# Optimization experiments

Measured on AMD Instinct MI355X. Metric: run time of the kernel, lower is better.

## Reference

```python
import jax, jax.numpy as jnp
import numpy as np

N = 50000      # nodes
E = 800000     # edges
D = 256        # hidden_dim (input node features)
A = 128        # attention_dim = attention_ratio * heads
H = 8          # heads
DK = A // H    # 16


def setup_inputs() -> dict:
    key = jax.random.key(0)
    ks = jax.random.split(key, 6)
    x = jax.random.normal(ks[0], (N, D), dtype=jnp.float32)
    # small weight scale keeps exp(pre) well-conditioned (module uses tiny const init)
    Wq = jax.random.normal(ks[1], (A, D), dtype=jnp.float32) * 0.02
    bq = jnp.full((A,), 0.01, dtype=jnp.float32)
    Wk = jax.random.normal(ks[2], (A, D), dtype=jnp.float32) * 0.02
    bk = jnp.full((A,), 0.01, dtype=jnp.float32)
    edge_index = jax.random.randint(ks[3], (2, E), 0, N, dtype=jnp.int32)
    # d0_index[1] holds the two node indices each duplicated edge score scatters to
    d0_index = jax.random.randint(ks[4], (2, 2 * E), 0, N, dtype=jnp.int32)
    return {"x": x, "Wq": Wq, "bq": bq, "Wk": Wk, "bk": bk,
            "edge_index": edge_index, "d0_index": d0_index}


def reference(x, Wq, bq, Wk, bk, edge_index, d0_index):
    # linear projections -> [N, H, DK]
    q = (x @ Wq.T + bq).reshape(N, H, DK)
    k = (x @ Wk.T + bk).reshape(N, H, DK)
    src, dst = edge_index[0], edge_index[1]
    q_i = q[src]   # [E, H, DK]
    k_j = k[dst]
    q_j = q[dst]
    k_i = k[src]
    # symmetrized scaled-dot attention score per edge/head
    pre = 0.5 * jnp.sum(q_i * k_j + q_j * k_i, axis=-1)  # [E, H]
    pre = jnp.mean(pre, axis=-1)                          # [E]
    diagA1 = jnp.exp(pre)
    # duplicate each edge score: (a, a, b, b, ...) == torch (view(-1,1)*ones(E,2)).view(-1)
    edge_score_per_node = jnp.repeat(diagA1, 2)           # [2E]
    diagA0 = jax.ops.segment_sum(edge_score_per_node, d0_index[1], num_segments=N)
    return diagA0, diagA1
```

## Files before the change

### kernel.cpp

```cpp
#include <hip/hip_runtime.h>
#include <hip/hip_bf16.h>

#define N_NODES 50000
#define N_EDGES 800000
#define DIM 256
#define QKDIM 256
#define NB_T  391
#define CAP   6144
#define CAP2  2816
#define BPB2  44
#define ITEMS (2 * N_EDGES)
#define IPB   4096
#define EPB2  2048

typedef __bf16 bfrag  __attribute__((ext_vector_type(8)));
typedef __bf16 bf4    __attribute__((ext_vector_type(4)));
typedef float  ffrag  __attribute__((ext_vector_type(4)));
typedef float  f2     __attribute__((ext_vector_type(2)));
typedef float  f4v    __attribute__((ext_vector_type(4)));

#define EP_PITCH 272

__global__ __launch_bounds__(256) void prep_bin(
    const float* __restrict__ Wq, const float* __restrict__ Wk,
    __bf16* __restrict__ Wb,
    const int* __restrict__ d0, unsigned int* __restrict__ rec,
    int* __restrict__ cur,
    const int* __restrict__ edge_index, uint2* __restrict__ rec2,
    int* __restrict__ cur2, int do_edges)
{
    __shared__ int lcnt[NB_T];
    __shared__ int lbase[NB_T];
    const int tid = threadIdx.x;
    const int gtid = blockIdx.x * 256 + tid;

    const int i4 = gtid * 4;
    if (i4 < 65536) {
        const float* s = (i4 < 32768) ? (Wq + i4) : (Wk + (i4 - 32768));
        const float4 v = *(const float4*)s;
        bf4 o;
        o[0] = (__bf16)v.x; o[1] = (__bf16)v.y; o[2] = (__bf16)v.z; o[3] = (__bf16)v.w;
        *(bf4*)(Wb + i4) = o;
    }

    for (int b = tid; b < NB_T; b += 256) lcnt[b] = 0;
    __syncthreads();
    const int base = blockIdx.x * IPB;
    int tg[16];
    #pragma unroll
    for (int r = 0; r < 16; ++r) {
        const int i = base + r * 256 + tid;
        tg[r] = (i < ITEMS) ? d0[i] : -1;
        if (tg[r] >= 0) atomicAdd(&lcnt[tg[r] >> 7], 1);
    }
    __syncthreads();
    for (int b = tid; b < NB_T; b += 256) {
        const int c = lcnt[b];
        lbase[b] = c ? atomicAdd(&cur[b], c) : 0;
    }
    __syncthreads();
    for (int b = tid; b < NB_T; b += 256) lcnt[b] = 0;
    __syncthreads();
    #pragma unroll
    for (int r = 0; r < 16; ++r) {
        if (tg[r] >= 0) {
            const int i = base + r * 256 + tid;
            const int b = tg[r] >> 7;
            const int off = atomicAdd(&lcnt[b], 1);
            rec[(size_t)b * CAP + lbase[b] + off] =
                ((unsigned int)(tg[r] & 127) << 20) | (unsigned int)(i >> 1);
        }
    }

    if (!do_edges) return;

    __syncthreads();
    for (int b = tid; b < NB_T; b += 256) lcnt[b] = 0;
    __syncthreads();
    const int ebase = blockIdx.x * EPB2;
    int es[8], ed[8];
    #pragma unroll
    for (int r = 0; r < 8; ++r) {
        const int e = ebase + r * 256 + tid;
        es[r] = (e < N_EDGES) ? edge_index[e] : -1;
        ed[r] = (e < N_EDGES) ? edge_index[N_EDGES + e] : 0;
        if (es[r] >= 0) atomicAdd(&lcnt[es[r] >> 7], 1);
    }
    __syncthreads();
    for (int b = tid; b < NB_T; b += 256) {
        const int c = lcnt[b];
        lbase[b] = c ? atomicAdd(&cur2[b], c) : 0;
    }
    __syncthreads();
    for (int b = tid; b < NB_T; b += 256) lcnt[b] = 0;
    __syncthreads();
    #pragma unroll
    for (int r = 0; r < 8; ++r) {
        if (es[r] >= 0) {
            const int e = ebase + r * 256 + tid;
            const int b = es[r] >> 7;
            const int off = atomicAdd(&lcnt[b], 1);
            const unsigned long long pk = (unsigned long long)(unsigned)es[r]
                | ((unsigned long long)(unsigned)ed[r] << 17)
                | ((unsigned long long)(unsigned)e << 34);
            rec2[(size_t)b * CAP2 + lbase[b] + off] =
                make_uint2((unsigned)pk, (unsigned)(pk >> 32));
        }
    }
}

__global__ __launch_bounds__(256) void proj_mfma(
    const float* __restrict__ x,
    const __bf16* __restrict__ Wb,
    const float* __restrict__ bq, const float* __restrict__ bk,
    unsigned char* __restrict__ qk8)
{
    __shared__ __bf16 As[64 * 256];

    const int tid  = threadIdx.x;
    const int wv   = tid >> 6;
    const int lane = tid & 63;
    const int m    = lane & 15;
    const int q    = lane >> 4;
    const int mbase = blockIdx.x * 64;

    {
        const int srow = tid >> 2;
        const int c4   = tid & 3;
        int grow = mbase + srow;
        grow = grow < N_NODES ? grow : N_NODES - 1;
        const float* xp = x + (size_t)grow * DIM;
        const int mt_ = srow >> 4, m_ = srow & 15;
        #pragma unroll
        for (int i = 0; i < 16; ++i) {
            const int k = c4 * 4 + 16 * i;
            const f4v v = __builtin_nontemporal_load((const f4v*)(xp + k));
            bf4 o;
            o[0] = (__bf16)v[0]; o[1] = (__bf16)v[1];
            o[2] = (__bf16)v[2]; o[3] = (__bf16)v[3];
            const int seg = (k >> 5) * 4 + mt_;
            const int ln  = ((k >> 3) & 3) * 16 + m_;
            *(bf4*)(As + seg * 512 + ln * 8 + (k & 7)) = o;
        }
    }
    __syncthreads();

    ffrag acc[4][4] = {};

    #pragma unroll
    for (int h = 0; h < 2; ++h) {
        bfrag b[4][4];
        #pragma unroll
        for (int sp = 0; sp < 4; ++sp)
            #pragma unroll
            for (int nt = 0; nt < 4; ++nt) {
                const int col = wv * 64 + nt * 16 + m;
                b[sp][nt] = *(const bfrag*)(Wb + (size_t)col * DIM
                                            + 32 * (4 * h + sp) + 8 * q);
            }
        #pragma unroll
        for (int sp = 0; sp < 4; ++sp) {
            bfrag a[4];
            #pragma unroll
            for (int mt = 0; mt < 4; ++mt)
                a[mt] = *(const bfrag*)(As + ((4 * h + sp) * 4 + mt) * 512 + lane * 8);
            #pragma unroll
            for (int mt = 0; mt < 4; ++mt)
                #pragma unroll
                for (int nt = 0; nt < 4; ++nt)
                    acc[mt][nt] = __builtin_amdgcn_mfma_f32_16x16x32_bf16(
                                      a[mt], b[sp][nt], acc[mt][nt], 0, 0, 0);
        }
    }

    __syncthreads();
    unsigned char* ep = (unsigned char*)As;
    #pragma unroll
    for (int nt = 0; nt < 4; ++nt) {
        const int col  = wv * 64 + nt * 16 + m;
        const float bias = (col < 128) ? bq[col] : bk[col - 128];
        #pragma unroll
        for (int mt = 0; mt < 4; ++mt) {
            #pragma unroll
            for (int r = 0; r < 4; ++r) {
                const int rl = mt * 16 + q * 4 + r;
                const float v = acc[mt][nt][r] + bias;
                const int pk = __builtin_amdgcn_cvt_pk_fp8_f32(v, v, 0, false);
                ep[rl * EP_PITCH + col] = (unsigned char)(pk & 0xFF);
            }
        }
    }
    __syncthreads();
    {
        const int rl = tid >> 2;
        const int ch = tid & 3;
        const int grow = mbase + rl;
        if (grow < N_NODES) {
            const uint4* s4 = (const uint4*)(ep + rl * EP_PITCH + ch * 64);
            const uint4 t0 = s4[0], t1 = s4[1], t2 = s4[2], t3 = s4[3];
            uint4* g = (uint4*)(qk8 + (size_t)grow * QKDIM + ch * 64);
            g[0] = t0; g[1] = t1; g[2] = t2; g[3] = t3;
        }
    }
}

__global__ __launch_bounds__(256) void edge_compute(
    const unsigned char* __restrict__ qk8,
    const uint2* __restrict__ rec2, const int* __restrict__ cur2,
    float* __restrict__ out)
{
    const int b = blockIdx.x / BPB2;
    const int c = blockIdx.x - b * BPB2;
    const int lane = threadIdx.x & 63;
    const int g = lane >> 2;
    const int j = lane & 3;
    const int idx = c * 64 + ((threadIdx.x >> 6) << 4) + g;

    if (idx >= cur2[b]) return;

    const uint2 rw = rec2[(size_t)b * CAP2 + idx];
    const unsigned long long pk = ((unsigned long long)rw.y << 32) | rw.x;
    const int src = (int)(pk & 0x1FFFF);
    const int dst = (int)((pk >> 17) & 0x1FFFF);
    const int e   = (int)(pk >> 34);

    const uint4* rs = (const uint4*)(qk8 + (size_t)src * QKDIM + 64 * j);
    const uint4* rd = (const uint4*)(qk8 + (size_t)dst * QKDIM + 64 * ((j + 2) & 3));

    uint4 a[4], bb[4];
    #pragma unroll
    for (int i = 0; i < 4; ++i) { a[i] = rs[i]; bb[i] = rd[i]; }

    f2 acc = {0.f, 0.f};
    #pragma unroll
    for (int i = 0; i < 4; ++i) {
        const unsigned int* ua = (const unsigned int*)&a[i];
        const unsigned int* ub = (const unsigned int*)&bb[i];
        #pragma unroll
        for (int t = 0; t < 4; ++t) {
            const f2 x0 = __builtin_amdgcn_cvt_pk_f32_fp8(ua[t], false);
            const f2 y0 = __builtin_amdgcn_cvt_pk_f32_fp8(ub[t], false);
            const f2 x1 = __builtin_amdgcn_cvt_pk_f32_fp8(ua[t], true);
            const f2 y1 = __builtin_amdgcn_cvt_pk_f32_fp8(ub[t], true);
            acc += x0 * y0;
            acc += x1 * y1;
        }
    }
    float p = acc[0] + acc[1];
    p += __shfl_xor(p, 1, 64);
    p += __shfl_xor(p, 2, 64);

    if (j == 0)
        out[N_NODES + e] = __expf(p * 0.0625f);
}

__global__ __launch_bounds__(256) void edge_direct(
    const unsigned char* __restrict__ qk8,
    const int* __restrict__ edge_index,
    float* __restrict__ out)
{
    const int wave = (blockIdx.x * blockDim.x + threadIdx.x) >> 6;
    const int lane = threadIdx.x & 63;
    const int g = lane >> 2, j = lane & 3;
    const int e = wave * 16 + g;

    const int src = __builtin_nontemporal_load(edge_index + e);
    const int dst = __builtin_nontemporal_load(edge_index + N_EDGES + e);

    const uint4* rs = (const uint4*)(qk8 + (size_t)src * QKDIM + 64 * j);
    const uint4* rd = (const uint4*)(qk8 + (size_t)dst * QKDIM + 64 * ((j + 2) & 3));

    uint4 a[4], b[4];
    #pragma unroll
    for (int i = 0; i < 4; ++i) { a[i] = rs[i]; b[i] = rd[i]; }

    f2 acc = {0.f, 0.f};
    #pragma unroll
    for (int i = 0; i < 4; ++i) {
        const unsigned int* ua = (const unsigned int*)&a[i];
        const unsigned int* ub = (const unsigned int*)&b[i];
        #pragma unroll
        for (int t = 0; t < 4; ++t) {
            const f2 x0 = __builtin_amdgcn_cvt_pk_f32_fp8(ua[t], false);
            const f2 y0 = __builtin_amdgcn_cvt_pk_f32_fp8(ub[t], false);
            const f2 x1 = __builtin_amdgcn_cvt_pk_f32_fp8(ua[t], true);
            const f2 y1 = __builtin_amdgcn_cvt_pk_f32_fp8(ub[t], true);
            acc += x0 * y0;
            acc += x1 * y1;
        }
    }
    float p = acc[0] + acc[1];
    p += __shfl_xor(p, 1, 64);
    p += __shfl_xor(p, 2, 64);

    if (j == 0)
        out[N_NODES + e] = __expf(p * 0.0625f);
}

__global__ __launch_bounds__(1024) void phase_scatter(
    const unsigned int* __restrict__ rec, const int* __restrict__ cur,
    float* __restrict__ out)
{
    __shared__ float acc[128];
    const int b = blockIdx.x;
    const int tid = threadIdx.x;
    if (tid < 128) acc[tid] = 0.f;
    __syncthreads();

    const int cnt = cur[b];
    const unsigned int* rb = rec + (size_t)b * CAP;
    for (int i = tid; i < cnt; i += 1024) {
        const unsigned int r = rb[i];
        const float v = out[N_NODES + (r & 0xFFFFF)];
        atomicAdd(&acc[r >> 20], v);
    }
    __syncthreads();

    if (tid < 128) {
        const int n = b * 128 + tid;
        if (n < N_NODES) out[n] = acc[tid];
    }
}

extern "C" void kernel_launch(void* const* d_in, const int* in_sizes, int n_in,
                              void* d_out, int out_size, void* d_ws, size_t ws_size,
                              hipStream_t stream) {
    const float* x  = (const float*)d_in[0];
    const float* Wq = (const float*)d_in[1];
    const float* bq = (const float*)d_in[2];
    const float* Wk = (const float*)d_in[3];
    const float* bk = (const float*)d_in[4];
    const int* edge_index = (const int*)d_in[5];
    const int* d0 = (const int*)d_in[6] + 2 * N_EDGES;
    float* out = (float*)d_out;

    char* w = (char*)d_ws;
    unsigned char* qk8 = (unsigned char*)w;  w += (size_t)N_NODES * QKDIM;
    __bf16* Wb = (__bf16*)w;                 w += 131072;
    unsigned int* rec = (unsigned int*)w;    w += (size_t)NB_T * CAP * 4;
    uint2* rec2 = (uint2*)w;                 w += (size_t)NB_T * CAP2 * 8;
    int* cur = (int*)w;                      w += 4096;

    const size_t need = (size_t)(w - (char*)d_ws);
    const int use_sorted = (ws_size >= need) ? 1 : 0;
    int* cur2 = cur + NB_T;

    hipMemsetAsync(cur, 0, 2 * NB_T * sizeof(int), stream);
    prep_bin<<<NB_T, 256, 0, stream>>>(Wq, Wk, Wb, d0, rec, cur,
                                       edge_index, rec2, cur2, use_sorted);
    proj_mfma<<<(N_NODES + 63) / 64, 256, 0, stream>>>(x, Wb, bq, bk, qk8);
    if (use_sorted)
        edge_compute<<<NB_T * BPB2, 256, 0, stream>>>(qk8, rec2, cur2, out);
    else
        edge_direct<<<N_EDGES / 64, 256, 0, stream>>>(qk8, edge_index, out);
    phase_scatter<<<NB_T, 1024, 0, stream>>>(rec, cur, out);
}
```

Baseline: 219.1 us.

## Finer edge bins, persistent per-bin edge blocks, interleaved row loads, per-wave scatter accumulators

Edges are binned by source node into 64-node bins instead of 128-node bins. The edge kernel now runs two persistent blocks per bin that loop over half the bin each, replacing many short-lived blocks. Row loads are interleaved so the four lanes of a group read adjacent 16-byte chunks, which should coalesce better. The node scatter keeps a separate shared-memory accumulator per wave to cut atomic contention, at the cost of more LDS and a final 16-way reduction. CAP grows and CAP2 shrinks, which raises the risk of bin overflow if a bin exceeds its capacity.

After: 227.1 us. 1.04x slower.

```diff
diff --git a/kernel.cpp b/kernel.cpp
--- a/kernel.cpp
+++ b/kernel.cpp
@@ -6,9 +6,9 @@
 #define DIM 256
 #define QKDIM 256
 #define NB_T  391
-#define CAP   6144
-#define CAP2  2816
-#define BPB2  44
+#define CAP   8192
+#define NB2   782
+#define CAP2  1536
 #define ITEMS (2 * N_EDGES)
 #define IPB   4096
 #define EPB2  2048
@@ -29,8 +29,8 @@
     const int* __restrict__ edge_index, uint2* __restrict__ rec2,
     int* __restrict__ cur2, int do_edges)
 {
-    __shared__ int lcnt[NB_T];
-    __shared__ int lbase[NB_T];
+    __shared__ int lcnt[NB2];
+    __shared__ int lbase[NB2];
     const int tid = threadIdx.x;
     const int gtid = blockIdx.x * 256 + tid;
 
@@ -75,7 +75,7 @@
     if (!do_edges) return;
 
     __syncthreads();
-    for (int b = tid; b < NB_T; b += 256) lcnt[b] = 0;
+    for (int b = tid; b < NB2; b += 256) lcnt[b] = 0;
     __syncthreads();
     const int ebase = blockIdx.x * EPB2;
     int es[8], ed[8];
@@ -84,21 +84,21 @@
         const int e = ebase + r * 256 + tid;
         es[r] = (e < N_EDGES) ? edge_index[e] : -1;
         ed[r] = (e < N_EDGES) ? edge_index[N_EDGES + e] : 0;
-        if (es[r] >= 0) atomicAdd(&lcnt[es[r] >> 7], 1);
-    }
-    __syncthreads();
-    for (int b = tid; b < NB_T; b += 256) {
+        if (es[r] >= 0) atomicAdd(&lcnt[es[r] >> 6], 1);
+    }
+    __syncthreads();
+    for (int b = tid; b < NB2; b += 256) {
         const int c = lcnt[b];
         lbase[b] = c ? atomicAdd(&cur2[b], c) : 0;
     }
     __syncthreads();
-    for (int b = tid; b < NB_T; b += 256) lcnt[b] = 0;
+    for (int b = tid; b < NB2; b += 256) lcnt[b] = 0;
     __syncthreads();
     #pragma unroll
     for (int r = 0; r < 8; ++r) {
         if (es[r] >= 0) {
             const int e = ebase + r * 256 + tid;
-            const int b = es[r] >> 7;
+            const int b = es[r] >> 6;
             const int off = atomicAdd(&lcnt[b], 1);
             const unsigned long long pk = (unsigned long long)(unsigned)es[r]
                 | ((unsigned long long)(unsigned)ed[r] << 17)
@@ -209,33 +209,88 @@
     const uint2* __restrict__ rec2, const int* __restrict__ cur2,
     float* __restrict__ out)
 {
-    const int b = blockIdx.x / BPB2;
-    const int c = blockIdx.x - b * BPB2;
+    const int B = blockIdx.x;
+    const int b = B >> 1, h = B & 1;
+    const int cnt = cur2[b];
+    const int mid = (cnt + 1) >> 1;
+    const int lo = h ? mid : 0;
+    const int hi = h ? cnt : mid;
+
     const int lane = threadIdx.x & 63;
+    const int wid  = threadIdx.x >> 6;
     const int g = lane >> 2;
     const int j = lane & 3;
-    const int idx = c * 64 + ((threadIdx.x >> 6) << 4) + g;
-
-    if (idx >= cur2[b]) return;
-
-    const uint2 rw = rec2[(size_t)b * CAP2 + idx];
-    const unsigned long long pk = ((unsigned long long)rw.y << 32) | rw.x;
-    const int src = (int)(pk & 0x1FFFF);
-    const int dst = (int)((pk >> 17) & 0x1FFFF);
-    const int e   = (int)(pk >> 34);
-
-    const uint4* rs = (const uint4*)(qk8 + (size_t)src * QKDIM + 64 * j);
-    const uint4* rd = (const uint4*)(qk8 + (size_t)dst * QKDIM + 64 * ((j + 2) & 3));
-
-    uint4 a[4], bb[4];
-    #pragma unroll
-    for (int i = 0; i < 4; ++i) { a[i] = rs[i]; bb[i] = rd[i]; }
+    const int slot = wid * 16 + g;
+
+    const uint2* rb = rec2 + (size_t)b * CAP2;
+
+    for (int it = lo + slot; it < hi; it += 64) {
+        const uint2 rw = rb[it];
+        const unsigned long long pk = ((unsigned long long)rw.y << 32) | rw.x;
+        const int src = (int)(pk & 0x1FFFF);
+        const int dst = (int)((pk >> 17) & 0x1FFFF);
+        const int e   = (int)(pk >> 34);
+
+        const uint4* rs = (const uint4*)(qk8 + (size_t)src * QKDIM);
+        const uint4* rd = (const uint4*)(qk8 + (size_t)dst * QKDIM);
+
+        uint4 a[4], bb[4];
+        #pragma unroll
+        for (int i = 0; i < 4; ++i) a[i] = rs[4 * i + j];
+        #pragma unroll
+        for (int i = 0; i < 4; ++i) bb[i] = rd[4 * ((i + 2) & 3) + j];
+
+        f2 acc = {0.f, 0.f};
+        #pragma unroll
+        for (int i = 0; i < 4; ++i) {
+            const unsigned int* ua = (const unsigned int*)&a[i];
+            const unsigned int* ub = (const unsigned int*)&bb[i];
+            #pragma unroll
+            for (int t = 0; t < 4; ++t) {
+                const f2 x0 = __builtin_amdgcn_cvt_pk_f32_fp8(ua[t], false);
+                const f2 y0 = __builtin_amdgcn_cvt_pk_f32_fp8(ub[t], false);
+                const f2 x1 = __builtin_amdgcn_cvt_pk_f32_fp8(ua[t], true);
+                const f2 y1 = __builtin_amdgcn_cvt_pk_f32_fp8(ub[t], true);
+                acc += x0 * y0;
+                acc += x1 * y1;
+            }
+        }
+        float p = acc[0] + acc[1];
+        p += __shfl_xor(p, 1, 64);
+        p += __shfl_xor(p, 2, 64);
+
+        if (j == 0)
+            out[N_NODES + e] = __expf(p * 0.0625f);
+    }
+}
+
+__global__ __launch_bounds__(256) void edge_direct(
+    const unsigned char* __restrict__ qk8,
+    const int* __restrict__ edge_index,
+    float* __restrict__ out)
+{
+    const int wave = (blockIdx.x * blockDim.x + threadIdx.x) >> 6;
+    const int lane = threadIdx.x & 63;
+    const int g = lane >> 2, j = lane & 3;
+    const int e = wave * 16 + g;
+
+    const int src = __builtin_nontemporal_load(edge_index + e);
+    const int dst = __builtin_nontemporal_load(edge_index + N_EDGES + e);
+
+    const uint4* rs = (const uint4*)(qk8 + (size_t)src * QKDIM);
+    const uint4* rd = (const uint4*)(qk8 + (size_t)dst * QKDIM);
+
+    uint4 a[4], b[4];
+    #pragma unroll
+    for (int i = 0; i < 4; ++i) a[i] = rs[4 * i + j];
+    #pragma unroll
+    for (int i = 0; i < 4; ++i) b[i] = rd[4 * ((i + 2) & 3) + j];
 
     f2 acc = {0.f, 0.f};
     #pragma unroll
     for (int i = 0; i < 4; ++i) {
         const unsigned int* ua = (const unsigned int*)&a[i];
-        const unsigned int* ub = (const unsigned int*)&bb[i];
+        const unsigned int* ub = (const unsigned int*)&b[i];
         #pragma unroll
         for (int t = 0; t < 4; ++t) {
             const f2 x0 = __builtin_amdgcn_cvt_pk_f32_fp8(ua[t], false);
@@ -254,57 +309,15 @@
         out[N_NODES + e] = __expf(p * 0.0625f);
 }
 
-__global__ __launch_bounds__(256) void edge_direct(
-    const unsigned char* __restrict__ qk8,
-    const int* __restrict__ edge_index,
-    float* __restrict__ out)
-{
-    const int wave = (blockIdx.x * blockDim.x + threadIdx.x) >> 6;
-    const int lane = threadIdx.x & 63;
-    const int g = lane >> 2, j = lane & 3;
-    const int e = wave * 16 + g;
-
-    const int src = __builtin_nontemporal_load(edge_index + e);
-    const int dst = __builtin_nontemporal_load(edge_index + N_EDGES + e);
-
-    const uint4* rs = (const uint4*)(qk8 + (size_t)src * QKDIM + 64 * j);
-    const uint4* rd = (const uint4*)(qk8 + (size_t)dst * QKDIM + 64 * ((j + 2) & 3));
-
-    uint4 a[4], b[4];
-    #pragma unroll
-    for (int i = 0; i < 4; ++i) { a[i] = rs[i]; b[i] = rd[i]; }
-
-    f2 acc = {0.f, 0.f};
-    #pragma unroll
-    for (int i = 0; i < 4; ++i) {
-        const unsigned int* ua = (const unsigned int*)&a[i];
-        const unsigned int* ub = (const unsigned int*)&b[i];
-        #pragma unroll
-        for (int t = 0; t < 4; ++t) {
-            const f2 x0 = __builtin_amdgcn_cvt_pk_f32_fp8(ua[t], false);
-            const f2 y0 = __builtin_amdgcn_cvt_pk_f32_fp8(ub[t], false);
-            const f2 x1 = __builtin_amdgcn_cvt_pk_f32_fp8(ua[t], true);
-            const f2 y1 = __builtin_amdgcn_cvt_pk_f32_fp8(ub[t], true);
-            acc += x0 * y0;
-            acc += x1 * y1;
-        }
-    }
-    float p = acc[0] + acc[1];
-    p += __shfl_xor(p, 1, 64);
-    p += __shfl_xor(p, 2, 64);
-
-    if (j == 0)
-        out[N_NODES + e] = __expf(p * 0.0625f);
-}
-
 __global__ __launch_bounds__(1024) void phase_scatter(
     const unsigned int* __restrict__ rec, const int* __restrict__ cur,
     float* __restrict__ out)
 {
-    __shared__ float acc[128];
+    __shared__ float acc[16][128];
     const int b = blockIdx.x;
     const int tid = threadIdx.x;
-    if (tid < 128) acc[tid] = 0.f;
+    const int wid = tid >> 6;
+    for (int i = tid; i < 16 * 128; i += 1024) ((float*)acc)[i] = 0.f;
     __syncthreads();
 
     const int cnt = cur[b];
@@ -312,13 +325,16 @@
     for (int i = tid; i < cnt; i += 1024) {
         const unsigned int r = rb[i];
         const float v = out[N_NODES + (r & 0xFFFFF)];
-        atomicAdd(&acc[r >> 20], v);
+        atomicAdd(&acc[wid][r >> 20], v);
     }
     __syncthreads();
 
     if (tid < 128) {
+        float s = 0.f;
+        #pragma unroll
+        for (int w = 0; w < 16; ++w) s += acc[w][tid];
         const int n = b * 128 + tid;
-        if (n < N_NODES) out[n] = acc[tid];
+        if (n < N_NODES) out[n] = s;
     }
 }
 
@@ -338,19 +354,19 @@
     unsigned char* qk8 = (unsigned char*)w;  w += (size_t)N_NODES * QKDIM;
     __bf16* Wb = (__bf16*)w;                 w += 131072;
     unsigned int* rec = (unsigned int*)w;    w += (size_t)NB_T * CAP * 4;
-    uint2* rec2 = (uint2*)w;                 w += (size_t)NB_T * CAP2 * 8;
-    int* cur = (int*)w;                      w += 4096;
+    uint2* rec2 = (uint2*)w;                 w += (size_t)NB2 * CAP2 * 8;
+    int* cur = (int*)w;                      w += 8192;
 
     const size_t need = (size_t)(w - (char*)d_ws);
     const int use_sorted = (ws_size >= need) ? 1 : 0;
     int* cur2 = cur + NB_T;
 
-    hipMemsetAsync(cur, 0, 2 * NB_T * sizeof(int), stream);
+    hipMemsetAsync(cur, 0, (NB_T + NB2) * sizeof(int), stream);
     prep_bin<<<NB_T, 256, 0, stream>>>(Wq, Wk, Wb, d0, rec, cur,
                                        edge_index, rec2, cur2, use_sorted);
     proj_mfma<<<(N_NODES + 63) / 64, 256, 0, stream>>>(x, Wb, bq, bk, qk8);
     if (use_sorted)
-        edge_compute<<<NB_T * BPB2, 256, 0, stream>>>(qk8, rec2, cur2, out);
+        edge_compute<<<2 * NB2, 256, 0, stream>>>(qk8, rec2, cur2, out);
     else
         edge_direct<<<N_EDGES / 64, 256, 0, stream>>>(qk8, edge_index, out);
     phase_scatter<<<NB_T, 1024, 0, stream>>>(rec, cur, out);
```
